# Kernel optimization log

Hardware: AMD Instinct MI355X
Metric: run time of the kernel (lower is better)

Reference implementation:

```python
import jax, jax.numpy as jnp
import numpy as np

B, S, HID = 2, 1024, 4096
NH, NKV = 32, 8            # query heads, kv heads (GQA)
D = HID // NH              # head_size = 128
G = NH // NKV              # groups = 4
SCALE = D ** -0.5


def setup_inputs() -> dict:
    key = jax.random.key(0)
    k1, k2, k3 = jax.random.split(key, 3)
    hidden_states = jax.random.normal(k1, (B, S, HID), dtype=jnp.float32)
    # rotary tables: dim=head_size, base=10000 (PositionRotaryEmbedding.static)
    inv_freq = 1.0 / (10000.0 ** (jnp.arange(0, D, 2, dtype=jnp.float32) / D))  # [D/2]
    t = jnp.arange(S, dtype=jnp.float32)
    freqs = jnp.outer(t, inv_freq)                       # [S, D/2]
    cos, sin = jnp.cos(freqs), jnp.sin(freqs)
    wqkv = jax.random.normal(k2, (HID, (NH + 2 * NKV) * D), dtype=jnp.float32) * (HID ** -0.5)
    wo = jax.random.normal(k3, (NH * D, HID), dtype=jnp.float32) * (HID ** -0.5)
    return {"hidden_states": hidden_states, "cos": cos, "sin": sin, "wqkv": wqkv, "wo": wo}


def _rope(x, cos, sin):
    # interleaved-pair rotary (TGI convention); x: [B,S,H,D], cos/sin: [S,D/2]
    x1, x2 = x[..., 0::2], x[..., 1::2]
    c = cos[None, :, None, :]
    s = sin[None, :, None, :]
    r1 = x1 * c - x2 * s
    r2 = x1 * s + x2 * c
    return jnp.stack([r1, r2], axis=-1).reshape(x.shape)


def reference(hidden_states, cos, sin, wqkv, wo):
    qkv = hidden_states @ wqkv                                  # [B,S,(NH+2*NKV)*D]
    q = qkv[..., : NH * D].reshape(B, S, NH, D)
    k = qkv[..., NH * D : (NH + NKV) * D].reshape(B, S, NKV, D)
    v = qkv[..., (NH + NKV) * D :].reshape(B, S, NKV, D)
    q = _rope(q, cos, sin)
    k = _rope(k, cos, sin)
    # GQA: group query heads over kv heads
    qg = q.reshape(B, S, NKV, G, D)
    scores = jnp.einsum('bqkgd,bskd->bkgqs', qg, k) * SCALE     # [B,NKV,G,S,S]
    causal = jnp.tril(jnp.ones((S, S), dtype=bool))
    scores = jnp.where(causal, scores, jnp.finfo(scores.dtype).min)
    p = jax.nn.softmax(scores, axis=-1)
    out = jnp.einsum('bkgqs,bskd->bqkgd', p, v).reshape(B, S, NH * D)
    return out @ wo                                             # [B,S,HID]
```

## Files before the change

### kernel.cpp

```cpp
#include <hip/hip_runtime.h>
#include <hip/hip_bf16.h>

typedef __bf16 bf16;
typedef __attribute__((ext_vector_type(2))) __bf16 bf16x2;
typedef __attribute__((ext_vector_type(4))) __bf16 bf16x4;
typedef __attribute__((ext_vector_type(8))) __bf16 bf16x8;
typedef __attribute__((ext_vector_type(4))) float f32x4;

#define NB 2
#define SEQ 1024
#define HIDN 4096
#define NH 32
#define NKV 8
#define DH 128
#define QKV_N 6144
static constexpr float SCALE = 0.08838834764831845f;

#define MFMA(a, b, c) __builtin_amdgcn_mfma_f32_16x16x32_bf16((a), (b), (c), 0, 0, 0)

__device__ __forceinline__ void async16(const void* g, void* l) {
  __builtin_amdgcn_global_load_lds(
      (const __attribute__((address_space(1))) unsigned int*)g,
      (__attribute__((address_space(3))) unsigned int*)l,
      16, 0, 0);
}

__device__ __forceinline__ void barrier_raw() {
  asm volatile("" ::: "memory");
  __builtin_amdgcn_s_barrier();
  asm volatile("" ::: "memory");
}
#define VMCNT(n) asm volatile("s_waitcnt vmcnt(" #n ")" ::: "memory")

__global__ __launch_bounds__(256) void cvt_f32_bf16(const float* __restrict__ src,
                                                    bf16* __restrict__ dst, int n4) {
  int i = blockIdx.x * 256 + threadIdx.x;
  if (i >= n4) return;
  const float4 v = ((const float4*)src)[i];
  bf16x4 o = {(bf16)v.x, (bf16)v.y, (bf16)v.z, (bf16)v.w};
  ((bf16x4*)dst)[i] = o;
}

__global__ __launch_bounds__(256) void transpose_cvt(const float* __restrict__ src,
                                                     bf16* __restrict__ dst, int R, int C) {
  __shared__ float tl[32][33];
  const int j0 = blockIdx.x * 32, i0 = blockIdx.y * 32;
  const int tr = threadIdx.x >> 5, tc = threadIdx.x & 31;
#pragma unroll
  for (int p = 0; p < 4; ++p)
    tl[tr + p * 8][tc] = src[(size_t)(i0 + tr + p * 8) * C + j0 + tc];
  __syncthreads();
#pragma unroll
  for (int p = 0; p < 4; ++p)
    dst[(size_t)(j0 + tr + p * 8) * R + i0 + tc] = (bf16)tl[tc][tr + p * 8];
}

template <int BN, int OUT_BF16>
__global__ __launch_bounds__(512, 2) void gemm_dp(const bf16* __restrict__ A,
                                                  const bf16* __restrict__ BT,
                                                  void* __restrict__ Cout,
                                                  int N, int K) {
  extern __shared__ char smem[];
  constexpr int CA = 128 * 32 * 2;
  constexpr int CB = BN * 32 * 2;
  constexpr int BUF = CA + CB;
  constexpr int LTOT = 1 + BN / 128;
  constexpr int FN = BN / 64;
  constexpr int FNH = FN / 2;
  const int t = threadIdx.x, lane = t & 63, w = t >> 6;
  const int l16 = lane & 15, lq = lane >> 4;
  const int wm = w >> 2, wn = w & 3;

  const int nwg = gridDim.x;
  const int lin = ((int)blockIdx.x & 7) * (nwg >> 3) + ((int)blockIdx.x >> 3);
  const int m0 = (lin & 15) * 128;
  const int n0 = (lin >> 4) * BN;

  const int sslot = (t & 3) ^ ((t >> 3) & 3);
  const bf16* gsrc[LTOT];
  gsrc[0] = A + (size_t)(m0 + (t >> 2)) * K + sslot * 8;
#pragma unroll
  for (int u = 1; u < LTOT; ++u)
    gsrc[u] = BT + (size_t)(n0 + (u - 1) * 128 + (t >> 2)) * K + sslot * 8;

  int abyte[4], bbyte[FN];
#pragma unroll
  for (int f = 0; f < 4; ++f) {
    const int r = wm * 64 + f * 16 + l16;
    abyte[f] = r * 64 + ((lq ^ ((r >> 1) & 3)) << 4);
  }
#pragma unroll
  for (int j = 0; j < FN; ++j) {
    const int r = wn * (BN / 4) + j * 16 + l16;
    bbyte[j] = CA + r * 64 + ((lq ^ ((r >> 1) & 3)) << 4);
  }

  auto stage_unit = [&](int kt, int u) {
    char* d = smem + (kt & 3) * BUF + u * 8192 + t * 16;
    async16(gsrc[u] + (size_t)kt * 32, d);
  };

  f32x4 acc[4][FN] = {};
  const int NT = K >> 5;

#pragma unroll
  for (int kt = 0; kt < 3; ++kt)
#pragma unroll
    for (int u = 0; u < LTOT; ++u) stage_unit(kt, u);
  if constexpr (LTOT == 4) { VMCNT(8); } else { VMCNT(6); }
  barrier_raw();

  for (int kt = 0; kt < NT; ++kt) {
    const char* buf = smem + (kt & 3) * BUF;
    const bool pf = (kt + 3 < NT);
    bf16x8 af[4], bf0[FNH];
#pragma unroll
    for (int f = 0; f < 4; ++f) af[f] = *(const bf16x8*)(buf + abyte[f]);
#pragma unroll
    for (int j = 0; j < FNH; ++j) bf0[j] = *(const bf16x8*)(buf + bbyte[j]);
    if (pf) {
      stage_unit(kt + 3, 0);
      stage_unit(kt + 3, 1);
    }
    barrier_raw();
    __builtin_amdgcn_s_setprio(1);
#pragma unroll
    for (int f = 0; f < 4; ++f)
#pragma unroll
      for (int j = 0; j < FNH; ++j) acc[f][j] = MFMA(af[f], bf0[j], acc[f][j]);
    __builtin_amdgcn_s_setprio(0);
    bf16x8 bf1[FN - FNH];
#pragma unroll
    for (int j = 0; j < FN - FNH; ++j) bf1[j] = *(const bf16x8*)(buf + bbyte[FNH + j]);
    if (pf) {
#pragma unroll
      for (int u = 2; u < LTOT; ++u) stage_unit(kt + 3, u);
    }
    if (pf) {
      if constexpr (LTOT == 4) { VMCNT(8); } else { VMCNT(6); }
    } else if (kt + 2 < NT) {
      if constexpr (LTOT == 4) { VMCNT(4); } else { VMCNT(3); }
    } else {
      VMCNT(0);
    }
    barrier_raw();
    __builtin_amdgcn_s_setprio(1);
#pragma unroll
    for (int f = 0; f < 4; ++f)
#pragma unroll
      for (int j = 0; j < FN - FNH; ++j)
        acc[f][FNH + j] = MFMA(af[f], bf1[j], acc[f][FNH + j]);
    __builtin_amdgcn_s_setprio(0);
  }

#pragma unroll
  for (int f = 0; f < 4; ++f)
#pragma unroll
    for (int j = 0; j < FN; ++j)
#pragma unroll
      for (int r = 0; r < 4; ++r) {
        const int row = m0 + wm * 64 + f * 16 + lq * 4 + r;
        const int col = n0 + wn * (BN / 4) + j * 16 + l16;
        if (OUT_BF16)
          ((bf16*)Cout)[(size_t)row * N + col] = (bf16)acc[f][j][r];
        else
          ((float*)Cout)[(size_t)row * N + col] = acc[f][j][r];
      }
}

__global__ __launch_bounds__(256) void rope_reshape(const bf16* __restrict__ qkv,
                                                    const float* __restrict__ cosp,
                                                    const float* __restrict__ sinp,
                                                    bf16* __restrict__ Qo,
                                                    bf16* __restrict__ Ko,
                                                    bf16* __restrict__ VTo) {
  const int row = blockIdx.x;
  const int b = row >> 10, s = row & 1023;
  const bf16* src = qkv + (size_t)row * QKV_N;
  for (int p = threadIdx.x; p < QKV_N / 2; p += 256) {
    const int col = p * 2;
    bf16x2 x = *(const bf16x2*)&src[col];
    const float x1 = (float)x.x, x2 = (float)x.y;
    if (col < 4096) {
      const int h = col >> 7, d = col & 127, i = (col & 127) >> 1;
      const float c = cosp[s * 64 + i], sn = sinp[s * 64 + i];
      bf16x2 o = {(bf16)((x1 * c - x2 * sn) * SCALE), (bf16)((x1 * sn + x2 * c) * SCALE)};
      *(bf16x2*)&Qo[((size_t)(b * NH + h) * SEQ + s) * DH + d] = o;
    } else if (col < 5120) {
      const int idx = col - 4096;
      const int kvh = idx >> 7, d = idx & 127, i = (idx & 127) >> 1;
      const float c = cosp[s * 64 + i], sn = sinp[s * 64 + i];
      bf16x2 o = {(bf16)(x1 * c - x2 * sn), (bf16)(x1 * sn + x2 * c)};
      *(bf16x2*)&Ko[((size_t)(b * NKV + kvh) * SEQ + s) * DH + d] = o;
    } else {
      const int idx = col - 5120;
      const int kvh = idx >> 7, d = idx & 127;
      bf16* vbase = VTo + ((size_t)(b * NKV + kvh) * DH + d) * SEQ + s;
      vbase[0] = x.x;
      vbase[SEQ] = x.y;
    }
  }
}

__global__ __launch_bounds__(512, 2) void flash_attn(const bf16* __restrict__ Q,
                                                     const bf16* __restrict__ K,
                                                     const bf16* __restrict__ VT,
                                                     bf16* __restrict__ O) {
  extern __shared__ char smem[];
  const int t = threadIdx.x, lane = t & 63, w = t >> 6;
  const int l16 = lane & 15, lq = lane >> 4;
  const int p = blockIdx.x;
  const int b = p >> 7, h = (p >> 2) & 31, Tb = p & 3;
  const int kvh = h >> 2;

  const bf16* Qb = Q + (size_t)(b * NH + h) * SEQ * DH;
  const bf16* Kb = K + (size_t)(b * NKV + kvh) * SEQ * DH;
  const bf16* Vb = VT + (size_t)(b * NKV + kvh) * DH * SEQ;

  const int qrA = Tb * 128 + w * 16;
  const int qrB = (7 - Tb) * 128 + w * 16;
  const int nAw = (qrA >> 6) + 1;
  const int nBw = (qrB >> 6) + 1;
  const int NT = 16 - 2 * Tb;

  bf16* plw = (bf16*)(smem + 98304) + w * (2 * 16 * 72);

  const bf16* kSrc = Kb + (size_t)(t >> 4) * DH + 8 * ((t & 15) ^ ((t >> 4) & 7));
  const bf16* vSrc = Vb + (size_t)(t >> 3) * SEQ + 8 * ((t & 7) ^ ((t >> 3) & 7));

  auto stage = [&](int kv) {
    char* bufb = smem + (kv % 3) * 32768;
    async16(kSrc + (size_t)(kv * 64) * DH, bufb + t * 16);
    async16(kSrc + (size_t)(kv * 64 + 32) * DH, bufb + 8192 + t * 16);
    async16(vSrc + kv * 64, bufb + 16384 + t * 16);
    async16(vSrc + (size_t)64 * SEQ + kv * 64, bufb + 24576 + t * 16);
  };

  int KX[4], VX[2];
#pragma unroll
  for (int kk = 0; kk < 4; ++kk) KX[kk] = ((kk * 4 + lq) ^ (l16 & 7)) << 4;
#pragma unroll
  for (int c = 0; c < 2; ++c) VX[c] = ((c * 4 + lq) ^ (l16 & 7)) << 4;

  bf16x8 qfA[4], qfB[4];
#pragma unroll
  for (int kk = 0; kk < 4; ++kk) {
    qfA[kk] = *(const bf16x8*)&Qb[(size_t)(qrA + l16) * DH + kk * 32 + lq * 8];
    qfB[kk] = *(const bf16x8*)&Qb[(size_t)(qrB + l16) * DH + kk * 32 + lq * 8];
  }

  f32x4 accA[8] = {}, accB[8] = {};
  float mA[4], lA[4], mB[4], lB[4];
#pragma unroll
  for (int r = 0; r < 4; ++r) {
    mA[r] = mB[r] = -INFINITY;
    lA[r] = lB[r] = 0.f;
  }

  auto finish = [&](f32x4(&s)[4], float(&m)[4], float(&l)[4], f32x4(&acc)[8], int slot,
                    bool mask, int kv, int qr) {
    if (mask) {
#pragma unroll
      for (int nt = 0; nt < 4; ++nt)
#pragma unroll
        for (int r = 0; r < 4; ++r)
          if (kv * 64 + nt * 16 + l16 > qr + lq * 4 + r) s[nt][r] = -INFINITY;
    }
#pragma unroll
    for (int r = 0; r < 4; ++r) {
      float mx = fmaxf(fmaxf(s[0][r], s[1][r]), fmaxf(s[2][r], s[3][r]));
#pragma unroll
      for (int off = 1; off < 16; off <<= 1) mx = fmaxf(mx, __shfl_xor(mx, off));
      const float mn = fmaxf(m[r], mx);
      const float corr = __expf(m[r] - mn);
      m[r] = mn;
      float ps = 0.f;
#pragma unroll
      for (int nt = 0; nt < 4; ++nt) {
        const float pv = __expf(s[nt][r] - mn);
        s[nt][r] = pv;
        ps += pv;
      }
#pragma unroll
      for (int off = 1; off < 16; off <<= 1) ps += __shfl_xor(ps, off);
      l[r] = l[r] * corr + ps;
#pragma unroll
      for (int j = 0; j < 8; ++j) acc[j][r] *= corr;
    }
#pragma unroll
    for (int nt = 0; nt < 4; ++nt)
#pragma unroll
      for (int r = 0; r < 4; ++r)
        plw[slot * 1152 + (lq * 4 + r) * 72 + nt * 16 + l16] = (bf16)s[nt][r];
  };

  stage(0);
  stage(1);
  VMCNT(4);
  barrier_raw();

  for (int kv = 0; kv < NT; ++kv) {
    const char* kbuf = smem + (kv % 3) * 32768;
    const char* vbuf = kbuf + 16384;
    if (kv + 2 < NT) stage(kv + 2);

    if (kv < nAw) {
      f32x4 sA[4] = {}, sB[4] = {};
      __builtin_amdgcn_s_setprio(1);
#pragma unroll
      for (int nt = 0; nt < 4; ++nt) {
        const char* kr = kbuf + (nt * 16 + l16) * 256;
        bf16x8 k0 = *(const bf16x8*)(kr + KX[0]);
        bf16x8 k1 = *(const bf16x8*)(kr + KX[1]);
        bf16x8 k2 = *(const bf16x8*)(kr + KX[2]);
        bf16x8 k3 = *(const bf16x8*)(kr + KX[3]);
        sA[nt] = MFMA(qfA[0], k0, sA[nt]);
        sB[nt] = MFMA(qfB[0], k0, sB[nt]);
        sA[nt] = MFMA(qfA[1], k1, sA[nt]);
        sB[nt] = MFMA(qfB[1], k1, sB[nt]);
        sA[nt] = MFMA(qfA[2], k2, sA[nt]);
        sB[nt] = MFMA(qfB[2], k2, sB[nt]);
        sA[nt] = MFMA(qfA[3], k3, sA[nt]);
        sB[nt] = MFMA(qfB[3], k3, sB[nt]);
      }
      __builtin_amdgcn_s_setprio(0);
      finish(sA, mA, lA, accA, 0, kv == nAw - 1, kv, qrA);
      finish(sB, mB, lB, accB, 1, kv == nBw - 1, kv, qrB);
      bf16x8 pA0 = *(const bf16x8*)&plw[l16 * 72 + lq * 8];
      bf16x8 pA1 = *(const bf16x8*)&plw[l16 * 72 + 32 + lq * 8];
      bf16x8 pB0 = *(const bf16x8*)&plw[1152 + l16 * 72 + lq * 8];
      bf16x8 pB1 = *(const bf16x8*)&plw[1152 + l16 * 72 + 32 + lq * 8];
      __builtin_amdgcn_s_setprio(1);
#pragma unroll
      for (int j = 0; j < 8; ++j) {
        const char* vr = vbuf + (j * 16 + l16) * 128;
        bf16x8 v0 = *(const bf16x8*)(vr + VX[0]);
        bf16x8 v1 = *(const bf16x8*)(vr + VX[1]);
        accA[j] = MFMA(pA0, v0, accA[j]);
        accB[j] = MFMA(pB0, v0, accB[j]);
        accA[j] = MFMA(pA1, v1, accA[j]);
        accB[j] = MFMA(pB1, v1, accB[j]);
      }
      __builtin_amdgcn_s_setprio(0);
    } else if (kv < nBw) {
      f32x4 sB[4] = {};
      __builtin_amdgcn_s_setprio(1);
#pragma unroll
      for (int nt = 0; nt < 4; ++nt) {
        const char* kr = kbuf + (nt * 16 + l16) * 256;
        bf16x8 k0 = *(const bf16x8*)(kr + KX[0]);
        bf16x8 k1 = *(const bf16x8*)(kr + KX[1]);
        bf16x8 k2 = *(const bf16x8*)(kr + KX[2]);
        bf16x8 k3 = *(const bf16x8*)(kr + KX[3]);
        sB[nt] = MFMA(qfB[0], k0, sB[nt]);
        sB[nt] = MFMA(qfB[1], k1, sB[nt]);
        sB[nt] = MFMA(qfB[2], k2, sB[nt]);
        sB[nt] = MFMA(qfB[3], k3, sB[nt]);
      }
      __builtin_amdgcn_s_setprio(0);
      finish(sB, mB, lB, accB, 1, kv == nBw - 1, kv, qrB);
      bf16x8 pB0 = *(const bf16x8*)&plw[1152 + l16 * 72 + lq * 8];
      bf16x8 pB1 = *(const bf16x8*)&plw[1152 + l16 * 72 + 32 + lq * 8];
      __builtin_amdgcn_s_setprio(1);
#pragma unroll
      for (int j = 0; j < 8; ++j) {
        const char* vr = vbuf + (j * 16 + l16) * 128;
        bf16x8 v0 = *(const bf16x8*)(vr + VX[0]);
        bf16x8 v1 = *(const bf16x8*)(vr + VX[1]);
        accB[j] = MFMA(pB0, v0, accB[j]);
        accB[j] = MFMA(pB1, v1, accB[j]);
      }
      __builtin_amdgcn_s_setprio(0);
    }

    if (kv + 2 < NT) { VMCNT(4); } else { VMCNT(0); }
    barrier_raw();
  }

  auto wout = [&](f32x4(&acc)[8], float(&l)[4], int qr) {
#pragma unroll
    for (int r = 0; r < 4; ++r) {
      const float inv = 1.f / l[r];
      const size_t orow = ((size_t)b * SEQ + qr + lq * 4 + r) * HIDN + h * DH;
#pragma unroll
      for (int j = 0; j < 8; ++j) O[orow + j * 16 + l16] = (bf16)(acc[j][r] * inv);
    }
  };
  wout(accA, lA, qrA);
  wout(accB, lB, qrB);
}

extern "C" void kernel_launch(void* const* d_in, const int* in_sizes, int n_in,
                              void* d_out, int out_size, void* d_ws, size_t ws_size,
                              hipStream_t stream) {
  const float* hidden = (const float*)d_in[0];
  const float* cosp = (const float*)d_in[1];
  const float* sinp = (const float*)d_in[2];
  const float* wqkv = (const float*)d_in[3];
  const float* wo = (const float*)d_in[4];
  float* out = (float*)d_out;

  char* ws = (char*)d_ws;
  bf16* hiddenB = (bf16*)(ws);
  bf16* wqkvT  = (bf16*)(ws + 16777216);
  bf16* woT    = (bf16*)(ws + 67108864);
  bf16* qkvB   = (bf16*)(ws + 100663296);
  bf16* Qb     = (bf16*)(ws + 125829120);
  bf16* Kb     = (bf16*)(ws + 142606336);
  bf16* VTb    = (bf16*)(ws + 146800640);
  bf16* attnB  = hiddenB;

  cvt_f32_bf16<<<8192, 256, 0, stream>>>(hidden, hiddenB, 2097152);
  transpose_cvt<<<dim3(192, 128), 256, 0, stream>>>(wqkv, wqkvT, 4096, 6144);
  transpose_cvt<<<dim3(128, 128), 256, 0, stream>>>(wo, woT, 4096, 4096);
  gemm_dp<384, 1><<<dim3(256), 512, 131072, stream>>>(hiddenB, wqkvT, qkvB, 6144, 4096);
  rope_reshape<<<2048, 256, 0, stream>>>(qkvB, cosp, sinp, Qb, Kb, VTb);
  flash_attn<<<dim3(256), 512, 135168, stream>>>(Qb, Kb, VTb, attnB);
  gemm_dp<256, 0><<<dim3(256), 512, 98304, stream>>>(attnB, woT, out, 4096, 4096);
}
```

Measured before the change: 297.5 us.

## Load GEMM A operand directly from global into registers, stage only B in LDS

The GEMM kernel no longer stages the A tile through LDS. Each wave loads its A fragments straight from global memory into registers, double-buffered across k-tiles, while only the B tile is staged asynchronously into LDS with a 4-deep ring. The k-loop also merges the two half-MFMA phases into a single barrier per tile. This cuts LDS footprint and traffic and removes one barrier per tile, at the cost of uncoalesced per-lane global A loads, more register pressure, and reliance on cache hits for A reuse across waves.

```diff
diff --git a/kernel.cpp b/kernel.cpp
--- a/kernel.cpp
+++ b/kernel.cpp
@@ -56,17 +56,14 @@
 }
 
 template <int BN, int OUT_BF16>
-__global__ __launch_bounds__(512, 2) void gemm_dp(const bf16* __restrict__ A,
+__global__ __launch_bounds__(512, 2) void gemm_ag(const bf16* __restrict__ A,
                                                   const bf16* __restrict__ BT,
                                                   void* __restrict__ Cout,
                                                   int N, int K) {
   extern __shared__ char smem[];
-  constexpr int CA = 128 * 32 * 2;
   constexpr int CB = BN * 32 * 2;
-  constexpr int BUF = CA + CB;
-  constexpr int LTOT = 1 + BN / 128;
+  constexpr int LB = CB / 8192;
   constexpr int FN = BN / 64;
-  constexpr int FNH = FN / 2;
   const int t = threadIdx.x, lane = t & 63, w = t >> 6;
   const int l16 = lane & 15, lq = lane >> 4;
   const int wm = w >> 2, wn = w & 3;
@@ -76,81 +73,72 @@
   const int m0 = (lin & 15) * 128;
   const int n0 = (lin >> 4) * BN;
 
-  const int sslot = (t & 3) ^ ((t >> 3) & 3);
-  const bf16* gsrc[LTOT];
-  gsrc[0] = A + (size_t)(m0 + (t >> 2)) * K + sslot * 8;
-#pragma unroll
-  for (int u = 1; u < LTOT; ++u)
-    gsrc[u] = BT + (size_t)(n0 + (u - 1) * 128 + (t >> 2)) * K + sslot * 8;
-
-  int abyte[4], bbyte[FN];
-#pragma unroll
-  for (int f = 0; f < 4; ++f) {
-    const int r = wm * 64 + f * 16 + l16;
-    abyte[f] = r * 64 + ((lq ^ ((r >> 1) & 3)) << 4);
-  }
+  const int srow = t >> 2;
+  const int sslot = (t & 3) ^ ((srow >> 1) & 3);
+  const bf16* gB[LB];
+#pragma unroll
+  for (int u = 0; u < LB; ++u)
+    gB[u] = BT + (size_t)(n0 + u * 128 + srow) * K + sslot * 8;
+
+  const bf16* aptr[4];
+#pragma unroll
+  for (int f = 0; f < 4; ++f)
+    aptr[f] = A + (size_t)(m0 + wm * 64 + f * 16 + l16) * K + lq * 8;
+
+  int bbyte[FN];
 #pragma unroll
   for (int j = 0; j < FN; ++j) {
     const int r = wn * (BN / 4) + j * 16 + l16;
-    bbyte[j] = CA + r * 64 + ((lq ^ ((r >> 1) & 3)) << 4);
-  }
-
-  auto stage_unit = [&](int kt, int u) {
-    char* d = smem + (kt & 3) * BUF + u * 8192 + t * 16;
-    async16(gsrc[u] + (size_t)kt * 32, d);
+    bbyte[j] = r * 64 + ((lq ^ ((r >> 1) & 3)) << 4);
+  }
+
+  auto stageB = [&](int kt) {
+    char* d = smem + (kt & 3) * CB + t * 16;
+#pragma unroll
+    for (int u = 0; u < LB; ++u) async16(gB[u] + (size_t)kt * 32, d + u * 8192);
   };
 
   f32x4 acc[4][FN] = {};
   const int NT = K >> 5;
 
-#pragma unroll
-  for (int kt = 0; kt < 3; ++kt)
-#pragma unroll
-    for (int u = 0; u < LTOT; ++u) stage_unit(kt, u);
-  if constexpr (LTOT == 4) { VMCNT(8); } else { VMCNT(6); }
+  bf16x8 aCur[4], aNxt[4];
+
+  stageB(0);
+#pragma unroll
+  for (int f = 0; f < 4; ++f) aCur[f] = *(const bf16x8*)(aptr[f]);
+  stageB(1);
+  stageB(2);
+  if constexpr (LB == 3) { VMCNT(10); } else { VMCNT(8); }
   barrier_raw();
 
-  for (int kt = 0; kt < NT; ++kt) {
-    const char* buf = smem + (kt & 3) * BUF;
-    const bool pf = (kt + 3 < NT);
-    bf16x8 af[4], bf0[FNH];
-#pragma unroll
-    for (int f = 0; f < 4; ++f) af[f] = *(const bf16x8*)(buf + abyte[f]);
-#pragma unroll
-    for (int j = 0; j < FNH; ++j) bf0[j] = *(const bf16x8*)(buf + bbyte[j]);
-    if (pf) {
-      stage_unit(kt + 3, 0);
-      stage_unit(kt + 3, 1);
+  auto tile = [&](int kt, bf16x8(&aC)[4], bf16x8(&aN)[4]) {
+    const char* buf = smem + (kt & 3) * CB;
+    if (kt + 1 < NT) {
+#pragma unroll
+      for (int f = 0; f < 4; ++f)
+        aN[f] = *(const bf16x8*)(aptr[f] + (size_t)(kt + 1) * 32);
+    }
+    if (kt + 3 < NT) stageB(kt + 3);
+    bf16x8 bfr[FN];
+#pragma unroll
+    for (int j = 0; j < FN; ++j) bfr[j] = *(const bf16x8*)(buf + bbyte[j]);
+    if (kt + 3 < NT) {
+      if constexpr (LB == 3) { VMCNT(14); } else { VMCNT(12); }
+    } else {
+      VMCNT(0);
     }
     barrier_raw();
     __builtin_amdgcn_s_setprio(1);
 #pragma unroll
     for (int f = 0; f < 4; ++f)
 #pragma unroll
-      for (int j = 0; j < FNH; ++j) acc[f][j] = MFMA(af[f], bf0[j], acc[f][j]);
+      for (int j = 0; j < FN; ++j) acc[f][j] = MFMA(aC[f], bfr[j], acc[f][j]);
     __builtin_amdgcn_s_setprio(0);
-    bf16x8 bf1[FN - FNH];
-#pragma unroll
-    for (int j = 0; j < FN - FNH; ++j) bf1[j] = *(const bf16x8*)(buf + bbyte[FNH + j]);
-    if (pf) {
-#pragma unroll
-      for (int u = 2; u < LTOT; ++u) stage_unit(kt + 3, u);
-    }
-    if (pf) {
-      if constexpr (LTOT == 4) { VMCNT(8); } else { VMCNT(6); }
-    } else if (kt + 2 < NT) {
-      if constexpr (LTOT == 4) { VMCNT(4); } else { VMCNT(3); }
-    } else {
-      VMCNT(0);
-    }
-    barrier_raw();
-    __builtin_amdgcn_s_setprio(1);
-#pragma unroll
-    for (int f = 0; f < 4; ++f)
-#pragma unroll
-      for (int j = 0; j < FN - FNH; ++j)
-        acc[f][FNH + j] = MFMA(af[f], bf1[j], acc[f][FNH + j]);
-    __builtin_amdgcn_s_setprio(0);
+  };
+
+  for (int kt = 0; kt < NT; kt += 2) {
+    tile(kt, aCur, aNxt);
+    tile(kt + 1, aNxt, aCur);
   }
 
 #pragma unroll
@@ -413,8 +401,8 @@
   cvt_f32_bf16<<<8192, 256, 0, stream>>>(hidden, hiddenB, 2097152);
   transpose_cvt<<<dim3(192, 128), 256, 0, stream>>>(wqkv, wqkvT, 4096, 6144);
   transpose_cvt<<<dim3(128, 128), 256, 0, stream>>>(wo, woT, 4096, 4096);
-  gemm_dp<384, 1><<<dim3(256), 512, 131072, stream>>>(hiddenB, wqkvT, qkvB, 6144, 4096);
+  gemm_ag<384, 1><<<dim3(256), 512, 98304, stream>>>(hiddenB, wqkvT, qkvB, 6144, 4096);
   rope_reshape<<<2048, 256, 0, stream>>>(qkvB, cosp, sinp, Qb, Kb, VTb);
   flash_attn<<<dim3(256), 512, 135168, stream>>>(Qb, Kb, VTb, attnB);
-  gemm_dp<256, 0><<<dim3(256), 512, 98304, stream>>>(attnB, woT, out, 4096, 4096);
-}
+  gemm_ag<256, 0><<<dim3(256), 512, 65536, stream>>>(attnB, woT, out, 4096, 4096);
+}
```

Measured after the change: 427.5 us. +43.7%, slower.

## Double-buffer register fragments in GEMM to overlap LDS reads with MFMA

Applied to the files above, without the earlier changes.

Restructures the GEMM main loop so the A/B fragments for the next k-tile are read from LDS into a second register set while the MFMAs for the current tile run. The loop is unrolled by two to ping-pong between the register sets, and the two barriers per k-tile become one. This is meant to hide LDS read latency and cut synchronisation overhead, at the cost of more vector registers, which may pressure occupancy under the 512x2 launch bounds.

```diff
diff --git a/kernel.cpp b/kernel.cpp
--- a/kernel.cpp
+++ b/kernel.cpp
@@ -31,6 +31,7 @@
   asm volatile("" ::: "memory");
 }
 #define VMCNT(n) asm volatile("s_waitcnt vmcnt(" #n ")" ::: "memory")
+#define LGKM0 asm volatile("s_waitcnt lgkmcnt(0)" ::: "memory")
 
 __global__ __launch_bounds__(256) void cvt_f32_bf16(const float* __restrict__ src,
                                                     bf16* __restrict__ dst, int n4) {
@@ -56,17 +57,16 @@
 }
 
 template <int BN, int OUT_BF16>
-__global__ __launch_bounds__(512, 2) void gemm_dp(const bf16* __restrict__ A,
-                                                  const bf16* __restrict__ BT,
-                                                  void* __restrict__ Cout,
-                                                  int N, int K) {
+__global__ __launch_bounds__(512, 2) void gemm_dp2(const bf16* __restrict__ A,
+                                                   const bf16* __restrict__ BT,
+                                                   void* __restrict__ Cout,
+                                                   int N, int K) {
   extern __shared__ char smem[];
   constexpr int CA = 128 * 32 * 2;
   constexpr int CB = BN * 32 * 2;
   constexpr int BUF = CA + CB;
   constexpr int LTOT = 1 + BN / 128;
   constexpr int FN = BN / 64;
-  constexpr int FNH = FN / 2;
   const int t = threadIdx.x, lane = t & 63, w = t >> 6;
   const int l16 = lane & 15, lq = lane >> 4;
   const int wm = w >> 2, wn = w & 3;
@@ -95,62 +95,55 @@
     bbyte[j] = CA + r * 64 + ((lq ^ ((r >> 1) & 3)) << 4);
   }
 
-  auto stage_unit = [&](int kt, int u) {
-    char* d = smem + (kt & 3) * BUF + u * 8192 + t * 16;
-    async16(gsrc[u] + (size_t)kt * 32, d);
+  auto stage = [&](int kt) {
+    char* d = smem + (kt & 3) * BUF + t * 16;
+#pragma unroll
+    for (int u = 0; u < LTOT; ++u) async16(gsrc[u] + (size_t)kt * 32, d + u * 8192);
+  };
+  auto ldfrag = [&](int kt, bf16x8(&a)[4], bf16x8(&b)[FN]) {
+    const char* buf = smem + (kt & 3) * BUF;
+#pragma unroll
+    for (int f = 0; f < 4; ++f) a[f] = *(const bf16x8*)(buf + abyte[f]);
+#pragma unroll
+    for (int j = 0; j < FN; ++j) b[j] = *(const bf16x8*)(buf + bbyte[j]);
   };
 
   f32x4 acc[4][FN] = {};
   const int NT = K >> 5;
 
-#pragma unroll
-  for (int kt = 0; kt < 3; ++kt)
-#pragma unroll
-    for (int u = 0; u < LTOT; ++u) stage_unit(kt, u);
+  bf16x8 a0[4], a1[4], b0[FN], b1[FN];
+
+  stage(0);
+  stage(1);
+  stage(2);
   if constexpr (LTOT == 4) { VMCNT(8); } else { VMCNT(6); }
   barrier_raw();
-
-  for (int kt = 0; kt < NT; ++kt) {
-    const char* buf = smem + (kt & 3) * BUF;
-    const bool pf = (kt + 3 < NT);
-    bf16x8 af[4], bf0[FNH];
-#pragma unroll
-    for (int f = 0; f < 4; ++f) af[f] = *(const bf16x8*)(buf + abyte[f]);
-#pragma unroll
-    for (int j = 0; j < FNH; ++j) bf0[j] = *(const bf16x8*)(buf + bbyte[j]);
-    if (pf) {
-      stage_unit(kt + 3, 0);
-      stage_unit(kt + 3, 1);
-    }
-    barrier_raw();
-    __builtin_amdgcn_s_setprio(1);
-#pragma unroll
-    for (int f = 0; f < 4; ++f)
-#pragma unroll
-      for (int j = 0; j < FNH; ++j) acc[f][j] = MFMA(af[f], bf0[j], acc[f][j]);
-    __builtin_amdgcn_s_setprio(0);
-    bf16x8 bf1[FN - FNH];
-#pragma unroll
-    for (int j = 0; j < FN - FNH; ++j) bf1[j] = *(const bf16x8*)(buf + bbyte[FNH + j]);
-    if (pf) {
-#pragma unroll
-      for (int u = 2; u < LTOT; ++u) stage_unit(kt + 3, u);
-    }
-    if (pf) {
+  ldfrag(0, a0, b0);
+
+  auto tilestep = [&](int kt, bf16x8(&aC)[4], bf16x8(&bC)[FN], bf16x8(&aN)[4],
+                      bf16x8(&bN)[FN]) {
+    if (kt + 3 < NT) {
+      stage(kt + 3);
       if constexpr (LTOT == 4) { VMCNT(8); } else { VMCNT(6); }
     } else if (kt + 2 < NT) {
       if constexpr (LTOT == 4) { VMCNT(4); } else { VMCNT(3); }
-    } else {
+    } else if (kt + 1 < NT) {
       VMCNT(0);
     }
+    LGKM0;
     barrier_raw();
+    if (kt + 1 < NT) ldfrag(kt + 1, aN, bN);
     __builtin_amdgcn_s_setprio(1);
 #pragma unroll
     for (int f = 0; f < 4; ++f)
 #pragma unroll
-      for (int j = 0; j < FN - FNH; ++j)
-        acc[f][FNH + j] = MFMA(af[f], bf1[j], acc[f][FNH + j]);
+      for (int j = 0; j < FN; ++j) acc[f][j] = MFMA(aC[f], bC[j], acc[f][j]);
     __builtin_amdgcn_s_setprio(0);
+  };
+
+  for (int kt = 0; kt < NT; kt += 2) {
+    tilestep(kt, a0, b0, a1, b1);
+    tilestep(kt + 1, a1, b1, a0, b0);
   }
 
 #pragma unroll
@@ -413,8 +406,8 @@
   cvt_f32_bf16<<<8192, 256, 0, stream>>>(hidden, hiddenB, 2097152);
   transpose_cvt<<<dim3(192, 128), 256, 0, stream>>>(wqkv, wqkvT, 4096, 6144);
   transpose_cvt<<<dim3(128, 128), 256, 0, stream>>>(wo, woT, 4096, 4096);
-  gemm_dp<384, 1><<<dim3(256), 512, 131072, stream>>>(hiddenB, wqkvT, qkvB, 6144, 4096);
+  gemm_dp2<384, 1><<<dim3(256), 512, 131072, stream>>>(hiddenB, wqkvT, qkvB, 6144, 4096);
   rope_reshape<<<2048, 256, 0, stream>>>(qkvB, cosp, sinp, Qb, Kb, VTb);
   flash_attn<<<dim3(256), 512, 135168, stream>>>(Qb, Kb, VTb, attnB);
-  gemm_dp<256, 0><<<dim3(256), 512, 98304, stream>>>(attnB, woT, out, 4096, 4096);
-}
+  gemm_dp2<256, 0><<<dim3(256), 512, 98304, stream>>>(attnB, woT, out, 4096, 4096);
+}
```

After: 300.3 us. Within noise of the previous version (+1.0%).
